# Performance work log

Measured on AMD Instinct MI355X. Metric: run time of the kernel, lower is better.

The kernel has to match this reference:

```python
import jax, jax.numpy as jnp
import numpy as np

B, T, D_IN = 64, 365, 10
D_MODEL, N_HEAD, D_K = 256, 16, 8
D_HEAD = D_MODEL // N_HEAD  # 16, value head dim
MAX_POS = 365 + 2 * 30      # max_position + 2*max_temporal_shift = 425
BN_EPS = 1e-5


def _pos_table(n_pos, d, temp=1000.0):
    # standard sinusoidal table (frozen in the original via Embedding.from_pretrained)
    pos = np.arange(n_pos)[:, None].astype(np.float64)
    i = np.arange(d)[None, :]
    angle = pos / np.power(temp, 2 * (i // 2) / d)
    tab = np.where(i % 2 == 0, np.sin(angle), np.cos(angle))
    return jnp.asarray(tab, jnp.float32)

POS_TABLE = _pos_table(MAX_POS, D_MODEL)


def _linear_layer(x, W, b, g, beta):
    # LinearLayer = Linear -> BatchNorm1d (train-mode batch stats, per-feature) -> ReLU
    y = x @ W.T + b
    ax = tuple(range(y.ndim - 1))
    mu = y.mean(ax, keepdims=True)
    var = y.var(ax, keepdims=True)  # biased var, matches torch BN
    y = (y - mu) * jax.lax.rsqrt(var + BN_EPS) * g + beta
    return jax.nn.relu(y)


def _forward(positions, x, w1, b1, g1, e1, w2, b2, g2, e2, w3, b3, g3, e3,
             ws1, ws2, wi, bi, gi, ei, wk, bk, wq, bq, wm, bm, gm, em,
             wd1, bd1, gd1, ed1, wd2, bd2, gd2, ed2, wc, bc):
    # channel MLP encoder: 10 -> 64 -> 128 -> 256
    out = _linear_layer(x, w1, b1, g1, e1)
    out = _linear_layer(out, w2, b2, g2, e2)
    out = _linear_layer(out, w3, b3, g3, e3)                    # [B,T,256]
    # channel SE attention: avgpool over time, 2 linears (no bias), sigmoid, residual
    pooled = out.mean(axis=1, keepdims=True)                     # [B,1,256]
    att = jax.nn.sigmoid(jax.nn.relu(pooled @ ws1.T) @ ws2.T)    # [B,1,256]
    out = att * pooled + out                                     # broadcast residual
    # temporal attention block
    h = _linear_layer(out, wi, bi, gi, ei)                       # inconv -> [B,T,256]
    e = h + POS_TABLE[positions]                                 # add positional encoding
    q = (e @ wq.T + bq).reshape(B, T, N_HEAD, D_K)
    k = (e @ wk.T + bk).reshape(B, T, N_HEAD, D_K)
    v = e.reshape(B, T, N_HEAD, D_HEAD)
    # 'cross' attention: full score matrix, mean over key dim, softmax over query dim
    scores = jnp.einsum('bthd,bshd->bhts', q, k) / jnp.sqrt(jnp.float32(D_K))  # [B,H,T,T]
    scores = scores.mean(axis=-1)                                # [B,H,T]
    a = jax.nn.softmax(scores, axis=-1)                          # [B,H,T]
    y = jnp.einsum('bht,bthe->bhe', a, v).reshape(B, D_MODEL)    # [B,256]
    y = _linear_layer(y, wm, bm, gm, em)                         # mlp 256 -> 128
    # decoder: 128 -> 64 -> 32 -> num_classes
    z = _linear_layer(y, wd1, bd1, gd1, ed1)
    z = _linear_layer(z, wd2, bd2, gd2, ed2)
    return z @ wc.T + bc                                         # logits [B,10]


def setup_inputs():
    key = jax.random.key(0)
    ks = jax.random.split(key, 16)
    n = lambda i, sh: jax.random.normal(ks[i], sh, jnp.float32) * 0.05
    z, o = jnp.zeros, jnp.ones
    return {
        'x': jax.random.normal(ks[0], (B, T, D_IN), jnp.float32),
        'positions': jnp.sort(jax.random.randint(ks[1], (B, T), 0, MAX_POS), axis=-1),
        'w1': n(2, (64, D_IN)), 'b1': z(64), 'g1': o(64), 'e1': z(64),
        'w2': n(3, (128, 64)), 'b2': z(128), 'g2': o(128), 'e2': z(128),
        'w3': n(4, (256, 128)), 'b3': z(256), 'g3': o(256), 'e3': z(256),
        'ws1': n(5, (16, 256)), 'ws2': n(6, (256, 16)),
        'wi': n(7, (256, 256)), 'bi': z(256), 'gi': o(256), 'ei': z(256),
        'wk': n(8, (128, 256)), 'bk': z(128),
        'wq': n(9, (128, 256)), 'bq': z(128),
        'wm': n(10, (128, 256)), 'bm': z(128), 'gm': o(128), 'em': z(128),
        'wd1': n(11, (64, 128)), 'bd1': z(64), 'gd1': o(64), 'ed1': z(64),
        'wd2': n(12, (32, 64)), 'bd2': z(32), 'gd2': o(32), 'ed2': z(32),
        'wc': n(13, (10, 32)), 'bc': z(10),
    }


def reference(x, positions, w1, b1, g1, e1, w2, b2, g2, e2, w3, b3, g3, e3,
              ws1, ws2, wi, bi, gi, ei, wk, bk, wq, bq, wm, bm, gm, em,
              wd1, bd1, gd1, ed1, wd2, bd2, gd2, ed2, wc, bc):
    return _forward(positions, x, w1, b1, g1, e1, w2, b2, g2, e2, w3, b3, g3, e3,
                    ws1, ws2, wi, bi, gi, ei, wk, bk, wq, bq, wm, bm, gm, em,
                    wd1, bd1, gd1, ed1, wd2, bd2, gd2, ed2, wc, bc)
```

## Files before the change

kernel.cpp:

```cpp
#include <hip/hip_runtime.h>
#include <hip/hip_bf16.h>
#include <math.h>

#define TT 365
#define BT 23360
#define NPOS 425

typedef __hip_bfloat16 bf16;
typedef __attribute__((ext_vector_type(8))) short s16x8;
typedef __attribute__((ext_vector_type(4))) float f32x4;

__device__ __forceinline__ float b2f(bf16 v) { return __bfloat162float(v); }
__device__ __forceinline__ bf16  f2b(float v) { return __float2bfloat16(v); }
__device__ __forceinline__ float u2f(unsigned u) { return __uint_as_float(u); }
__device__ __forceinline__ short f2bs(float v) { bf16 h = __float2bfloat16(v); return *reinterpret_cast<short*>(&h); }
__device__ __forceinline__ void unpack8(uint4 raw, float* v) {
    v[0] = u2f(raw.x << 16); v[1] = u2f(raw.x & 0xffff0000u);
    v[2] = u2f(raw.y << 16); v[3] = u2f(raw.y & 0xffff0000u);
    v[4] = u2f(raw.z << 16); v[5] = u2f(raw.z & 0xffff0000u);
    v[6] = u2f(raw.w << 16); v[7] = u2f(raw.w & 0xffff0000u);
}

__global__ __launch_bounds__(256) void prep_kernel(
    float* __restrict__ stats, float* __restrict__ pooled, float* __restrict__ esum,
    const float* __restrict__ w2, const float* __restrict__ w3, const float* __restrict__ wi,
    const float* __restrict__ wq,
    bf16* __restrict__ whi, bf16* __restrict__ wlo, float* __restrict__ tab)
{
    int i = blockIdx.x * 256 + threadIdx.x;
    if (i < 2048)  { stats[i] = 0.f; return; }  i -= 2048;
    if (i < 16384) { pooled[i] = 0.f; return; } i -= 16384;
    if (i < 16384) { esum[i] = 0.f; return; }   i -= 16384;
    if (i < 139264) {
        float w;
        if      (i < 8192)   w = w2[i];
        else if (i < 40960)  w = w3[i - 8192];
        else if (i < 106496) w = wi[i - 40960];
        else                 w = wq[i - 106496];
        bf16 h = f2b(w);
        whi[i] = h;
        wlo[i] = f2b(w - b2f(h));
        return;
    } i -= 139264;
    if (i < 108800) {
        int c = i & 255, p = i >> 8;
        float e = (float)(2 * (c >> 1)) * (1.f / 256.f);
        float ang = (float)p * exp2f(-e * 9.96578428466209f);
        tab[i] = (c & 1) ? cosf(ang) : sinf(ang);
    }
}

__global__ __launch_bounds__(256) void gemm_l1_kernel(
    const float* __restrict__ x,
    const float* __restrict__ W, const float* __restrict__ bias,
    bf16* __restrict__ Y, float* __restrict__ stats)
{
    const int t  = threadIdx.x;
    const int tx = t & 15, ty = t >> 4;
    const int row0 = blockIdx.x * 64;
    __shared__ float As[64][17];
    __shared__ float Ws[16][65];
    __shared__ float red_s[4][64];
    __shared__ float red_q[4][64];
    float acc[4][4];
#pragma unroll
    for (int rr = 0; rr < 4; ++rr)
#pragma unroll
        for (int cc = 0; cc < 4; ++cc) acc[rr][cc] = 0.f;
#pragma unroll
    for (int i = 0; i < 4; ++i) {
        int idx = t + i * 256, r = idx >> 4, c = idx & 15;
        As[r][c] = (c < 10) ? x[(size_t)(row0 + r) * 10 + c] : 0.f;
    }
#pragma unroll
    for (int i = 0; i < 4; ++i) {
        int idx = t + i * 256, c = idx >> 4, kk = idx & 15;
        Ws[kk][c] = (kk < 10) ? W[(size_t)c * 10 + kk] : 0.f;
    }
    __syncthreads();
#pragma unroll
    for (int kk = 0; kk < 10; ++kk) {
        float a[4];
#pragma unroll
        for (int rr = 0; rr < 4; ++rr) a[rr] = As[ty * 4 + rr][kk];
#pragma unroll
        for (int cc = 0; cc < 4; ++cc) {
            float w = Ws[kk][cc * 16 + tx];
#pragma unroll
            for (int rr = 0; rr < 4; ++rr) acc[rr][cc] = fmaf(a[rr], w, acc[rr][cc]);
        }
    }
    float s_cc[4], q_cc[4];
#pragma unroll
    for (int cc = 0; cc < 4; ++cc) { s_cc[cc] = 0.f; q_cc[cc] = 0.f; }
#pragma unroll
    for (int rr = 0; rr < 4; ++rr) {
        int row = row0 + ty * 4 + rr;
#pragma unroll
        for (int cc = 0; cc < 4; ++cc) {
            int col = cc * 16 + tx;
            float v = acc[rr][cc] + bias[col];
            Y[(size_t)row * 64 + col] = f2b(v);
            s_cc[cc] += v; q_cc[cc] += v * v;
        }
    }
    int w = t >> 6;
#pragma unroll
    for (int cc = 0; cc < 4; ++cc) {
        float s = s_cc[cc], q = q_cc[cc];
        s += __shfl_xor(s, 16); q += __shfl_xor(q, 16);
        s += __shfl_xor(s, 32); q += __shfl_xor(q, 32);
        if ((t & 63) < 16) { red_s[w][cc * 16 + tx] = s; red_q[w][cc * 16 + tx] = q; }
    }
    __syncthreads();
    if (t < 64) {
        float s = red_s[0][t] + red_s[1][t] + red_s[2][t] + red_s[3][t];
        float q = red_q[0][t] + red_q[1][t] + red_q[2][t] + red_q[3][t];
        atomicAdd(&stats[t], s);
        atomicAdd(&stats[256 + t], q);
    }
}

template<int MODE, int K>
__global__ __launch_bounds__(256) void mfma_gemm(
    const bf16* __restrict__ A,
    const bf16* __restrict__ Whi, const bf16* __restrict__ Wlo,
    const float* __restrict__ bias,
    bf16* __restrict__ Y, int ldY, float* __restrict__ stats,
    const float* __restrict__ bnstats, const float* __restrict__ bng,
    const float* __restrict__ bnb, const float* __restrict__ sebuf)
{
    constexpr int KC = (K > 128) ? 128 : K;
    __shared__ s16x8 Wl[2][KC / 8][64];
    __shared__ float red_s[4][64];
    __shared__ float red_q[4][64];
    __shared__ float scb[MODE ? K : 1];
    __shared__ float shb[MODE ? K : 1];
    const int t = threadIdx.x, wave = t >> 6, lane = t & 63;
    const int n16 = lane & 15, quad = lane >> 4;
    const int m0 = blockIdx.x * 64 + wave * 16;
    const int col0 = blockIdx.y * 64;
    const int sc_ = t & 63, skg0 = t >> 6;
    const bf16* gh = Whi + (size_t)(col0 + sc_) * K;
    const bf16* gl = Wlo + (size_t)(col0 + sc_) * K;
#pragma unroll
    for (int kg = skg0; kg < KC / 8; kg += 4) {
        Wl[0][kg][sc_] = *(const s16x8*)(gh + kg * 8);
        Wl[1][kg][sc_] = *(const s16x8*)(gl + kg * 8);
    }
    if (MODE) {
        if (t < K) {
            float mu = bnstats[t] * (1.f / (float)BT);
            float var = bnstats[256 + t] * (1.f / (float)BT) - mu * mu;
            float sc = rsqrtf(var + 1e-5f) * bng[t];
            scb[t] = sc; shb[t] = bnb[t] - mu * sc;
        }
    }
    __syncthreads();
    const int arow = m0 + n16;
    const float* sev = (MODE == 2) ? (sebuf + (arow / TT) * 256) : nullptr;
    const bf16* Ap = A + (size_t)arow * K + quad * 8;
    s16x8 af[K / 32];
#pragma unroll
    for (int i = 0; i < K / 32; ++i) {
        s16x8 raw = *(const s16x8*)(Ap + i * 32);
        if (MODE) {
            int kb = i * 32 + quad * 8;
#pragma unroll
            for (int j = 0; j < 8; ++j) {
                float y = u2f(((unsigned)(unsigned short)raw[j]) << 16);
                float v = fmaxf(fmaf(y, scb[kb + j], shb[kb + j]), 0.f);
                if (MODE == 2) v += sev[kb + j];
                raw[j] = f2bs(v);
            }
        }
        af[i] = raw;
    }
    f32x4 acc[4];
    f32x4 zero = {0.f, 0.f, 0.f, 0.f};
#pragma unroll
    for (int ct = 0; ct < 4; ++ct) acc[ct] = zero;
#pragma unroll
    for (int kc = 0; kc < K; kc += KC) {
        if (kc) {
            __syncthreads();
#pragma unroll
            for (int kg = skg0; kg < KC / 8; kg += 4) {
                Wl[0][kg][sc_] = *(const s16x8*)(gh + kc + kg * 8);
                Wl[1][kg][sc_] = *(const s16x8*)(gl + kc + kg * 8);
            }
            __syncthreads();
        }
#pragma unroll
        for (int i = 0; i < KC / 32; ++i) {
            const int kgq = i * 4 + quad;
            const s16x8 a = af[(kc >> 5) + i];
#pragma unroll
            for (int ct = 0; ct < 4; ++ct) {
                s16x8 bl = Wl[1][kgq][ct * 16 + n16];
                s16x8 bh = Wl[0][kgq][ct * 16 + n16];
                acc[ct] = __builtin_amdgcn_mfma_f32_16x16x32_bf16(a, bl, acc[ct], 0, 0, 0);
                acc[ct] = __builtin_amdgcn_mfma_f32_16x16x32_bf16(a, bh, acc[ct], 0, 0, 0);
            }
        }
    }
#pragma unroll
    for (int ct = 0; ct < 4; ++ct) {
        int col = col0 + ct * 16 + n16;
        float bv = bias[col];
        float s = 0.f, q = 0.f;
#pragma unroll
        for (int r = 0; r < 4; ++r) {
            float v = acc[ct][r] + bv;
            int row = m0 + quad * 4 + r;
            Y[(size_t)row * ldY + col] = f2b(v);
            s += v; q += v * v;
        }
        s += __shfl_xor(s, 16); q += __shfl_xor(q, 16);
        s += __shfl_xor(s, 32); q += __shfl_xor(q, 32);
        if (quad == 0) { red_s[wave][ct * 16 + n16] = s; red_q[wave][ct * 16 + n16] = q; }
    }
    if (stats) {
        __syncthreads();
        if (t < 64) {
            float s = red_s[0][t] + red_s[1][t] + red_s[2][t] + red_s[3][t];
            float q = red_q[0][t] + red_q[1][t] + red_q[2][t] + red_q[3][t];
            atomicAdd(&stats[col0 + t], s);
            atomicAdd(&stats[256 + col0 + t], q);
        }
    }
}

__global__ __launch_bounds__(256) void pool_partial_kernel(
    const bf16* __restrict__ Y3, const float* __restrict__ stats,
    const float* __restrict__ g3, const float* __restrict__ e3,
    float* __restrict__ pooled)
{
    const int b = blockIdx.x, part = blockIdx.y, t = threadIdx.x;
    const int cg = t & 31, rs = t >> 5;
    __shared__ float scb[256], shb[256];
    __shared__ float pp[8][256];
    {
        float mu = stats[t] * (1.f / (float)BT);
        float var = stats[256 + t] * (1.f / (float)BT) - mu * mu;
        float sc = rsqrtf(var + 1e-5f) * g3[t];
        scb[t] = sc; shb[t] = e3[t] - mu * sc;
    }
    __syncthreads();
    float acc[8] = {0.f,0.f,0.f,0.f,0.f,0.f,0.f,0.f};
    const int r0 = part * 46;
#pragma unroll
    for (int i = 0; i < 6; ++i) {
        int l = rs + i * 8;
        int r = r0 + l;
        if (l < 46 && r < TT) {
            uint4 raw = *(const uint4*)(Y3 + ((size_t)b * TT + r) * 256 + cg * 8);
            float v[8];
            unpack8(raw, v);
#pragma unroll
            for (int j = 0; j < 8; ++j)
                acc[j] += fmaxf(fmaf(v[j], scb[cg * 8 + j], shb[cg * 8 + j]), 0.f);
        }
    }
#pragma unroll
    for (int j = 0; j < 8; ++j) pp[rs][cg * 8 + j] = acc[j];
    __syncthreads();
    float s = 0.f;
#pragma unroll
    for (int r = 0; r < 8; ++r) s += pp[r][t];
    atomicAdd(&pooled[b * 256 + t], s);
}

__global__ __launch_bounds__(256) void esum_kernel(const bf16* __restrict__ e,
                                                   float* __restrict__ esum)
{
    const int b = blockIdx.x, part = blockIdx.y, t = threadIdx.x;
    const int cg = t & 31, rs = t >> 5;
    __shared__ float pp[8][256];
    float acc[8] = {0.f,0.f,0.f,0.f,0.f,0.f,0.f,0.f};
    const int r0 = part * 46;
#pragma unroll
    for (int i = 0; i < 6; ++i) {
        int l = rs + i * 8;
        int r = r0 + l;
        if (l < 46 && r < TT) {
            uint4 raw = *(const uint4*)(e + ((size_t)b * TT + r) * 256 + cg * 8);
            float v[8];
            unpack8(raw, v);
#pragma unroll
            for (int j = 0; j < 8; ++j) acc[j] += v[j];
        }
    }
#pragma unroll
    for (int j = 0; j < 8; ++j) pp[rs][cg * 8 + j] = acc[j];
    __syncthreads();
    float s = 0.f;
#pragma unroll
    for (int r = 0; r < 8; ++r) s += pp[r][t];
    atomicAdd(&esum[b * 256 + t], s);
}

__global__ __launch_bounds__(256) void se_mlp_kernel(const float* __restrict__ pooled,
                                                     const float* __restrict__ ws1,
                                                     const float* __restrict__ ws2,
                                                     float* __restrict__ se) {
    int b = blockIdx.x, f = threadIdx.x;
    __shared__ float pl[256];
    __shared__ float hidden[16];
    float p = pooled[b * 256 + f] * (1.f / (float)TT);
    pl[f] = p;
    __syncthreads();
    if (f < 16) {
        float h = 0.f;
        for (int k2 = 0; k2 < 256; ++k2) h = fmaf(pl[k2], ws1[f * 256 + k2], h);
        hidden[f] = fmaxf(h, 0.f);
    }
    __syncthreads();
    float a = 0.f;
    for (int k2 = 0; k2 < 16; ++k2) a = fmaf(hidden[k2], ws2[f * 16 + k2], a);
    a = 1.f / (1.f + expf(-a));
    se[b * 256 + f] = a * p;
}

__global__ __launch_bounds__(256) void bnrelu8_kernel(
    const bf16* __restrict__ Y, const float* __restrict__ stats,
    const float* __restrict__ g, const float* __restrict__ beta,
    bf16* __restrict__ Out, const float* __restrict__ tab, const int* __restrict__ pos) {
    int i = (blockIdx.x * 256 + threadIdx.x) * 8;
    int col = i & 255, row = i >> 8;
    uint4 raw = *(const uint4*)(Y + i);
    float v[8];
    unpack8(raw, v);
    const float invM = 1.f / (float)BT;
    const float* tr = tab + pos[row] * 256 + col;
    bf16 tmp[8] __attribute__((aligned(16)));
#pragma unroll
    for (int j = 0; j < 8; ++j) {
        float mu  = stats[col + j] * invM;
        float var = stats[256 + col + j] * invM - mu * mu;
        float o = (v[j] - mu) * rsqrtf(var + 1e-5f) * g[col + j] + beta[col + j];
        tmp[j] = f2b(fmaxf(o, 0.f) + tr[j]);
    }
    *(uint4*)(Out + i) = *(const uint4*)tmp;
}

__global__ __launch_bounds__(64) void attn_kernel(
    const bf16* __restrict__ q, const bf16* __restrict__ e,
    const float* __restrict__ esum, const float* __restrict__ wk,
    const float* __restrict__ bk, float* __restrict__ yv)
{
    __shared__ float aw[368];
    const int b = blockIdx.x, h = blockIdx.y;
    const int lane = threadIdx.x;
    float4 es = *(const float4*)(esum + b * 256 + lane * 4);
    float ks[8];
#pragma unroll
    for (int d = 0; d < 8; ++d) {
        float4 wv = *(const float4*)(wk + (size_t)(h * 8 + d) * 256 + lane * 4);
        ks[d] = es.x * wv.x + es.y * wv.y + es.z * wv.z + es.w * wv.w;
    }
#pragma unroll
    for (int off = 1; off < 64; off <<= 1)
#pragma unroll
        for (int d = 0; d < 8; ++d) ks[d] += __shfl_xor(ks[d], off);
#pragma unroll
    for (int d = 0; d < 8; ++d) ks[d] += (float)TT * bk[h * 8 + d];
    const float scale = 1.f / (sqrtf(8.f) * (float)TT);
    const bf16* qb = q + (size_t)b * TT * 128 + h * 8;
    float sv[6];
    float m = -1e30f;
#pragma unroll
    for (int i = 0; i < 6; ++i) {
        int r = lane + i * 64;
        float s = -1e30f;
        if (r < TT) {
            uint4 raw = *(const uint4*)(qb + (size_t)r * 128);
            float v[8];
            unpack8(raw, v);
            float dot = 0.f;
#pragma unroll
            for (int j = 0; j < 8; ++j) dot = fmaf(v[j], ks[j], dot);
            s = dot * scale;
        }
        sv[i] = s;
        m = fmaxf(m, s);
    }
#pragma unroll
    for (int off = 1; off < 64; off <<= 1) m = fmaxf(m, __shfl_xor(m, off));
    float sum = 0.f;
#pragma unroll
    for (int i = 0; i < 6; ++i) {
        float ev = (sv[i] > -1e29f) ? expf(sv[i] - m) : 0.f;
        sv[i] = ev; sum += ev;
    }
#pragma unroll
    for (int off = 1; off < 64; off <<= 1) sum += __shfl_xor(sum, off);
    float inv = 1.f / sum;
#pragma unroll
    for (int i = 0; i < 6; ++i) {
        int r = lane + i * 64;
        if (r < TT) aw[r] = sv[i] * inv;
    }
    __syncthreads();
    const int half = lane & 1, rs = lane >> 1;
    float acc[8] = {0.f,0.f,0.f,0.f,0.f,0.f,0.f,0.f};
    const bf16* ebase = e + (size_t)b * TT * 256 + h * 16 + half * 8;
#pragma unroll
    for (int i = 0; i < 12; ++i) {
        int r = rs + i * 32;
        if (r < TT) {
            uint4 raw = *(const uint4*)(ebase + (size_t)r * 256);
            float v[8];
            unpack8(raw, v);
            float a = aw[r];
#pragma unroll
            for (int j = 0; j < 8; ++j) acc[j] = fmaf(a, v[j], acc[j]);
        }
    }
#pragma unroll
    for (int off = 2; off < 64; off <<= 1)
#pragma unroll
        for (int j = 0; j < 8; ++j) acc[j] += __shfl_xor(acc[j], off);
    if (lane < 2) {
        float* op = yv + b * 256 + h * 16 + half * 8;
#pragma unroll
        for (int j = 0; j < 8; ++j) op[j] = acc[j];
    }
}

__global__ __launch_bounds__(1024) void tail_kernel(
    const float* __restrict__ yv,
    const float* wm, const float* bm, const float* gm, const float* em,
    const float* wd1, const float* bd1, const float* gd1, const float* ed1,
    const float* wd2, const float* bd2, const float* gd2, const float* ed2,
    const float* wc, const float* bc, float* __restrict__ out)
{
    __shared__ float lds[12352];
    const int t = threadIdx.x;
    const int r = t & 63, cg = t >> 6;
    float* Xq  = lds;
    float* Wp  = lds + 4160;
    float* Z1t = lds;
    float* Wd1h = lds + 8192;
    float* Z2t = lds;
    float* Wd2 = lds + 4096;
    float* Z3t = lds + 6144;
    float* WcL = lds + 8192;

    float acc1[8] = {0.f,0.f,0.f,0.f,0.f,0.f,0.f,0.f};
    const int c01 = cg * 8;
    for (int p = 0; p < 4; ++p) {
        __syncthreads();
        for (int i = t; i < 4096; i += 1024) {
            int kk = i & 63, rr = i >> 6;
            Xq[kk * 65 + rr] = yv[rr * 256 + p * 64 + kk];
        }
        {
            const float4* wm4 = (const float4*)wm;
            float4* Wp4 = (float4*)Wp;
            for (int i = t; i < 2048; i += 1024) {
                int kk4 = i & 15, c = i >> 4;
                Wp4[c * 16 + kk4] = wm4[c * 64 + p * 16 + kk4];
            }
        }
        __syncthreads();
#pragma unroll 4
        for (int k4 = 0; k4 < 16; ++k4) {
            float xv[4];
#pragma unroll
            for (int j = 0; j < 4; ++j) xv[j] = Xq[(k4 * 4 + j) * 65 + r];
#pragma unroll
            for (int c = 0; c < 8; ++c) {
                float4 w = *(const float4*)(Wp + (c01 + c) * 64 + k4 * 4);
                acc1[c] = fmaf(xv[0], w.x, acc1[c]);
                acc1[c] = fmaf(xv[1], w.y, acc1[c]);
                acc1[c] = fmaf(xv[2], w.z, acc1[c]);
                acc1[c] = fmaf(xv[3], w.w, acc1[c]);
            }
        }
    }
    float z1v[8];
#pragma unroll
    for (int c = 0; c < 8; ++c) {
        float v = acc1[c] + bm[c01 + c];
        float s = v, q = v * v;
#pragma unroll
        for (int off = 1; off < 64; off <<= 1) { s += __shfl_xor(s, off); q += __shfl_xor(q, off); }
        float mu = s * (1.f / 64.f), var = q * (1.f / 64.f) - mu * mu;
        z1v[c] = fmaxf((v - mu) * rsqrtf(var + 1e-5f) * gm[c01 + c] + em[c01 + c], 0.f);
    }
    __syncthreads();
#pragma unroll
    for (int c = 0; c < 8; ++c) Z1t[(c01 + c) * 64 + r] = z1v[c];
    float acc2[4] = {0.f, 0.f, 0.f, 0.f};
    const int c02 = cg * 4;
    for (int ph = 0; ph < 2; ++ph) {
        __syncthreads();
        {
            const float4* s4 = (const float4*)wd1;
            float4* d4 = (float4*)Wd1h;
            int kk4 = t & 15, c = t >> 4;
            d4[c * 16 + kk4] = s4[c * 32 + ph * 16 + kk4];
        }
        __syncthreads();
#pragma unroll 4
        for (int k4 = 0; k4 < 16; ++k4) {
            float xv[4];
#pragma unroll
            for (int j = 0; j < 4; ++j) xv[j] = Z1t[(ph * 64 + k4 * 4 + j) * 64 + r];
#pragma unroll
            for (int c = 0; c < 4; ++c) {
                float4 w = *(const float4*)(Wd1h + (c02 + c) * 64 + k4 * 4);
                acc2[c] = fmaf(xv[0], w.x, acc2[c]);
                acc2[c] = fmaf(xv[1], w.y, acc2[c]);
                acc2[c] = fmaf(xv[2], w.z, acc2[c]);
                acc2[c] = fmaf(xv[3], w.w, acc2[c]);
            }
        }
    }
    float z2v[4];
#pragma unroll
    for (int c = 0; c < 4; ++c) {
        float v = acc2[c] + bd1[c02 + c];
        float s = v, q = v * v;
#pragma unroll
        for (int off = 1; off < 64; off <<= 1) { s += __shfl_xor(s, off); q += __shfl_xor(q, off); }
        float mu = s * (1.f / 64.f), var = q * (1.f / 64.f) - mu * mu;
        z2v[c] = fmaxf((v - mu) * rsqrtf(var + 1e-5f) * gd1[c02 + c] + ed1[c02 + c], 0.f);
    }
    __syncthreads();
#pragma unroll
    for (int c = 0; c < 4; ++c) Z2t[(c02 + c) * 64 + r] = z2v[c];
    {
        const float4* s4 = (const float4*)wd2;
        float4* d4 = (float4*)Wd2;
        if (t < 512) d4[t] = s4[t];
    }
    __syncthreads();
    float acc3[2] = {0.f, 0.f};
    const int c03 = cg * 2;
#pragma unroll 4
    for (int k4 = 0; k4 < 16; ++k4) {
        float xv[4];
#pragma unroll
        for (int j = 0; j < 4; ++j) xv[j] = Z2t[(k4 * 4 + j) * 64 + r];
#pragma unroll
        for (int c = 0; c < 2; ++c) {
            float4 w = *(const float4*)(Wd2 + (c03 + c) * 64 + k4 * 4);
            acc3[c] = fmaf(xv[0], w.x, acc3[c]);
            acc3[c] = fmaf(xv[1], w.y, acc3[c]);
            acc3[c] = fmaf(xv[2], w.z, acc3[c]);
            acc3[c] = fmaf(xv[3], w.w, acc3[c]);
        }
    }
#pragma unroll
    for (int c = 0; c < 2; ++c) {
        float v = acc3[c] + bd2[c03 + c];
        float s = v, q = v * v;
#pragma unroll
        for (int off = 1; off < 64; off <<= 1) { s += __shfl_xor(s, off); q += __shfl_xor(q, off); }
        float mu = s * (1.f / 64.f), var = q * (1.f / 64.f) - mu * mu;
        Z3t[(c03 + c) * 64 + r] = fmaxf((v - mu) * rsqrtf(var + 1e-5f) * gd2[c03 + c] + ed2[c03 + c], 0.f);
    }
    if (t < 80) ((float4*)WcL)[t] = ((const float4*)wc)[t];
    __syncthreads();
    if (t < 640) {
        int rr = t / 10, c = t % 10;
        float s = bc[c];
#pragma unroll
        for (int kk = 0; kk < 32; ++kk) s = fmaf(Z3t[kk * 64 + rr], WcL[c * 32 + kk], s);
        out[t] = s;
    }
}


extern "C" void kernel_launch(void* const* d_in, const int* in_sizes, int n_in,
                              void* d_out, int out_size, void* d_ws, size_t ws_size,
                              hipStream_t stream) {
    (void)in_sizes; (void)n_in; (void)out_size; (void)ws_size;
    const float* x  = (const float*)d_in[0];
    const int* pos  = (const int*)d_in[1];
    const float *w1 = (const float*)d_in[2],  *b1 = (const float*)d_in[3],
                *g1 = (const float*)d_in[4],  *e1 = (const float*)d_in[5];
    const float *w2 = (const float*)d_in[6],  *b2 = (const float*)d_in[7],
                *g2 = (const float*)d_in[8],  *e2 = (const float*)d_in[9];
    const float *w3 = (const float*)d_in[10], *b3 = (const float*)d_in[11],
                *g3 = (const float*)d_in[12], *e3 = (const float*)d_in[13];
    const float *ws1 = (const float*)d_in[14], *ws2 = (const float*)d_in[15];
    const float *wi = (const float*)d_in[16], *bi = (const float*)d_in[17],
                *gi = (const float*)d_in[18], *ei = (const float*)d_in[19];
    const float *wk = (const float*)d_in[20], *bk = (const float*)d_in[21];
    const float *wq = (const float*)d_in[22], *bq = (const float*)d_in[23];
    const float *wm = (const float*)d_in[24], *bm = (const float*)d_in[25],
                *gm = (const float*)d_in[26], *em = (const float*)d_in[27];
    const float *wd1 = (const float*)d_in[28], *bd1 = (const float*)d_in[29],
                *gd1 = (const float*)d_in[30], *ed1 = (const float*)d_in[31];
    const float *wd2 = (const float*)d_in[32], *bd2 = (const float*)d_in[33],
                *gd2 = (const float*)d_in[34], *ed2 = (const float*)d_in[35];
    const float *wc = (const float*)d_in[36], *bc = (const float*)d_in[37];
    float* out = (float*)d_out;

    char* w8 = (char*)d_ws;
    bf16*  actA   = (bf16*)(w8);
    bf16*  actB   = (bf16*)(w8 + 11960320);
    bf16*  whi    = (bf16*)(w8 + 23920640);
    bf16*  wlo    = (bf16*)(w8 + 24199168);
    float* tab    = (float*)(w8 + 24477696);
    float* stats  = (float*)(w8 + 24912896);
    float* pooled = (float*)(w8 + 24921088);
    float* sebuf  = (float*)(w8 + 24986624);
    float* esum   = (float*)(w8 + 25052160);
    float* yvb    = (float*)(w8 + 25117696);

    prep_kernel<<<1105, 256, 0, stream>>>(stats, pooled, esum, w2, w3, wi, wq, whi, wlo, tab);
    gemm_l1_kernel<<<365, 256, 0, stream>>>(x, w1, b1, actB, stats);
    mfma_gemm<1, 64><<<dim3(365, 2), 256, 0, stream>>>(actB, whi, wlo, b2,
                                                       actA, 128, stats + 512, stats, g1, e1, nullptr);
    mfma_gemm<1, 128><<<dim3(365, 4), 256, 0, stream>>>(actA, whi + 8192, wlo + 8192, b3,
                                                        actB, 256, stats + 1024, stats + 512, g2, e2, nullptr);
    pool_partial_kernel<<<dim3(64, 8), 256, 0, stream>>>(actB, stats + 1024, g3, e3, pooled);
    se_mlp_kernel<<<64, 256, 0, stream>>>(pooled, ws1, ws2, sebuf);
    mfma_gemm<2, 256><<<dim3(365, 4), 256, 0, stream>>>(actB, whi + 40960, wlo + 40960, bi,
                                                        actA, 256, stats + 1536, stats + 1024, g3, e3, sebuf);
    bnrelu8_kernel<<<BT * 256 / 2048, 256, 0, stream>>>(actA, stats + 1536, gi, ei, actB, tab, pos);
    esum_kernel<<<dim3(64, 8), 256, 0, stream>>>(actB, esum);
    mfma_gemm<0, 256><<<dim3(365, 2), 256, 0, stream>>>(actB, whi + 106496, wlo + 106496, bq,
                                                        actA, 128, nullptr, nullptr, nullptr, nullptr, nullptr);
    attn_kernel<<<dim3(64, 16), 64, 0, stream>>>(actA, actB, esum, wk, bk, yvb);
    tail_kernel<<<1, 1024, 0, stream>>>(yvb, wm, bm, gm, em, wd1, bd1, gd1, ed1,
                                        wd2, bd2, gd2, ed2, wc, bc, out);
}
```

Baseline: 318.6 us.

## Replace BN stat atomics with per-block partials and a reduction kernel

Each GEMM now writes its per-block column sums and sums of squares to a partials buffer instead of issuing atomicAdds. A new single-block reduction kernel turns these into BN scale/shift coefficients, so downstream kernels load precomputed coefficients rather than recomputing mean/var per thread. The tail kernel also drops its LDS weight staging and reads weights straight from global memory with wider unrolling. This trades atomic contention and redundant rsqrt work for four extra serial launches, each with a small single-block kernel.

Measured after the change: 395.1 us. 1.24x slower.

```diff
diff --git a/kernel.cpp b/kernel.cpp
--- a/kernel.cpp
+++ b/kernel.cpp
@@ -22,13 +22,12 @@
 }
 
 __global__ __launch_bounds__(256) void prep_kernel(
-    float* __restrict__ stats, float* __restrict__ pooled, float* __restrict__ esum,
+    float* __restrict__ pooled, float* __restrict__ esum,
     const float* __restrict__ w2, const float* __restrict__ w3, const float* __restrict__ wi,
     const float* __restrict__ wq,
     bf16* __restrict__ whi, bf16* __restrict__ wlo, float* __restrict__ tab)
 {
     int i = blockIdx.x * 256 + threadIdx.x;
-    if (i < 2048)  { stats[i] = 0.f; return; }  i -= 2048;
     if (i < 16384) { pooled[i] = 0.f; return; } i -= 16384;
     if (i < 16384) { esum[i] = 0.f; return; }   i -= 16384;
     if (i < 139264) {
@@ -50,10 +49,34 @@
     }
 }
 
+__global__ __launch_bounds__(512) void red_kernel(
+    const float* __restrict__ partials, const float* __restrict__ g,
+    const float* __restrict__ beta, float* __restrict__ coef, int Ncols)
+{
+    __shared__ float sums[512];
+    const int t = threadIdx.x;
+    const int c = t & 255;
+    const int off = (t >> 8) << 8;
+    float s = 0.f;
+    if (c < Ncols) {
+        const float* p = partials + off + c;
+        for (int r = 0; r < 365; ++r) s += p[r * 512];
+    }
+    sums[t] = s;
+    __syncthreads();
+    if (t < Ncols) {
+        float mu = sums[t] * (1.f / (float)BT);
+        float var = sums[256 + t] * (1.f / (float)BT) - mu * mu;
+        float sc = rsqrtf(var + 1e-5f) * g[t];
+        coef[t] = sc;
+        coef[256 + t] = beta[t] - mu * sc;
+    }
+}
+
 __global__ __launch_bounds__(256) void gemm_l1_kernel(
     const float* __restrict__ x,
     const float* __restrict__ W, const float* __restrict__ bias,
-    bf16* __restrict__ Y, float* __restrict__ stats)
+    bf16* __restrict__ Y, float* __restrict__ partials)
 {
     const int t  = threadIdx.x;
     const int tx = t & 15, ty = t >> 4;
@@ -114,10 +137,9 @@
     }
     __syncthreads();
     if (t < 64) {
-        float s = red_s[0][t] + red_s[1][t] + red_s[2][t] + red_s[3][t];
-        float q = red_q[0][t] + red_q[1][t] + red_q[2][t] + red_q[3][t];
-        atomicAdd(&stats[t], s);
-        atomicAdd(&stats[256 + t], q);
+        float* pr = partials + (size_t)blockIdx.x * 512;
+        pr[t]       = red_s[0][t] + red_s[1][t] + red_s[2][t] + red_s[3][t];
+        pr[256 + t] = red_q[0][t] + red_q[1][t] + red_q[2][t] + red_q[3][t];
     }
 }
 
@@ -126,9 +148,8 @@
     const bf16* __restrict__ A,
     const bf16* __restrict__ Whi, const bf16* __restrict__ Wlo,
     const float* __restrict__ bias,
-    bf16* __restrict__ Y, int ldY, float* __restrict__ stats,
-    const float* __restrict__ bnstats, const float* __restrict__ bng,
-    const float* __restrict__ bnb, const float* __restrict__ sebuf)
+    bf16* __restrict__ Y, int ldY, float* __restrict__ partials,
+    const float* __restrict__ coef, const float* __restrict__ sebuf)
 {
     constexpr int KC = (K > 128) ? 128 : K;
     __shared__ s16x8 Wl[2][KC / 8][64];
@@ -149,12 +170,7 @@
         Wl[1][kg][sc_] = *(const s16x8*)(gl + kg * 8);
     }
     if (MODE) {
-        if (t < K) {
-            float mu = bnstats[t] * (1.f / (float)BT);
-            float var = bnstats[256 + t] * (1.f / (float)BT) - mu * mu;
-            float sc = rsqrtf(var + 1e-5f) * bng[t];
-            scb[t] = sc; shb[t] = bnb[t] - mu * sc;
-        }
+        if (t < K) { scb[t] = coef[t]; shb[t] = coef[256 + t]; }
     }
     __syncthreads();
     const int arow = m0 + n16;
@@ -220,32 +236,25 @@
         s += __shfl_xor(s, 32); q += __shfl_xor(q, 32);
         if (quad == 0) { red_s[wave][ct * 16 + n16] = s; red_q[wave][ct * 16 + n16] = q; }
     }
-    if (stats) {
+    if (partials) {
         __syncthreads();
         if (t < 64) {
-            float s = red_s[0][t] + red_s[1][t] + red_s[2][t] + red_s[3][t];
-            float q = red_q[0][t] + red_q[1][t] + red_q[2][t] + red_q[3][t];
-            atomicAdd(&stats[col0 + t], s);
-            atomicAdd(&stats[256 + col0 + t], q);
+            float* pr = partials + (size_t)blockIdx.x * 512;
+            pr[col0 + t]       = red_s[0][t] + red_s[1][t] + red_s[2][t] + red_s[3][t];
+            pr[256 + col0 + t] = red_q[0][t] + red_q[1][t] + red_q[2][t] + red_q[3][t];
         }
     }
 }
 
 __global__ __launch_bounds__(256) void pool_partial_kernel(
-    const bf16* __restrict__ Y3, const float* __restrict__ stats,
-    const float* __restrict__ g3, const float* __restrict__ e3,
+    const bf16* __restrict__ Y3, const float* __restrict__ coef,
     float* __restrict__ pooled)
 {
     const int b = blockIdx.x, part = blockIdx.y, t = threadIdx.x;
     const int cg = t & 31, rs = t >> 5;
     __shared__ float scb[256], shb[256];
     __shared__ float pp[8][256];
-    {
-        float mu = stats[t] * (1.f / (float)BT);
-        float var = stats[256 + t] * (1.f / (float)BT) - mu * mu;
-        float sc = rsqrtf(var + 1e-5f) * g3[t];
-        scb[t] = sc; shb[t] = e3[t] - mu * sc;
-    }
+    scb[t] = coef[t]; shb[t] = coef[256 + t];
     __syncthreads();
     float acc[8] = {0.f,0.f,0.f,0.f,0.f,0.f,0.f,0.f};
     const int r0 = part * 46;
@@ -323,22 +332,18 @@
 }
 
 __global__ __launch_bounds__(256) void bnrelu8_kernel(
-    const bf16* __restrict__ Y, const float* __restrict__ stats,
-    const float* __restrict__ g, const float* __restrict__ beta,
+    const bf16* __restrict__ Y, const float* __restrict__ coef,
     bf16* __restrict__ Out, const float* __restrict__ tab, const int* __restrict__ pos) {
     int i = (blockIdx.x * 256 + threadIdx.x) * 8;
     int col = i & 255, row = i >> 8;
     uint4 raw = *(const uint4*)(Y + i);
     float v[8];
     unpack8(raw, v);
-    const float invM = 1.f / (float)BT;
     const float* tr = tab + pos[row] * 256 + col;
     bf16 tmp[8] __attribute__((aligned(16)));
 #pragma unroll
     for (int j = 0; j < 8; ++j) {
-        float mu  = stats[col + j] * invM;
-        float var = stats[256 + col + j] * invM - mu * mu;
-        float o = (v[j] - mu) * rsqrtf(var + 1e-5f) * g[col + j] + beta[col + j];
+        float o = fmaf(v[j], coef[col + j], coef[256 + col + j]);
         tmp[j] = f2b(fmaxf(o, 0.f) + tr[j]);
     }
     *(uint4*)(Out + i) = *(const uint4*)tmp;
@@ -430,145 +435,115 @@
 
 __global__ __launch_bounds__(1024) void tail_kernel(
     const float* __restrict__ yv,
-    const float* wm, const float* bm, const float* gm, const float* em,
-    const float* wd1, const float* bd1, const float* gd1, const float* ed1,
-    const float* wd2, const float* bd2, const float* gd2, const float* ed2,
-    const float* wc, const float* bc, float* __restrict__ out)
+    const float* __restrict__ wm, const float* __restrict__ bm,
+    const float* __restrict__ gm, const float* __restrict__ em,
+    const float* __restrict__ wd1, const float* __restrict__ bd1,
+    const float* __restrict__ gd1, const float* __restrict__ ed1,
+    const float* __restrict__ wd2, const float* __restrict__ bd2,
+    const float* __restrict__ gd2, const float* __restrict__ ed2,
+    const float* __restrict__ wc, const float* __restrict__ bc,
+    float* __restrict__ out)
 {
     __shared__ float lds[12352];
+    float* Xq  = lds;
+    float* Z1t = lds + 4160;
+    float* Z2t = lds;
+    float* Z3t = lds + 4160;
     const int t = threadIdx.x;
     const int r = t & 63, cg = t >> 6;
-    float* Xq  = lds;
-    float* Wp  = lds + 4160;
-    float* Z1t = lds;
-    float* Wd1h = lds + 8192;
-    float* Z2t = lds;
-    float* Wd2 = lds + 4096;
-    float* Z3t = lds + 6144;
-    float* WcL = lds + 8192;
+    const int cgu = __builtin_amdgcn_readfirstlane(cg);
 
     float acc1[8] = {0.f,0.f,0.f,0.f,0.f,0.f,0.f,0.f};
-    const int c01 = cg * 8;
     for (int p = 0; p < 4; ++p) {
         __syncthreads();
         for (int i = t; i < 4096; i += 1024) {
             int kk = i & 63, rr = i >> 6;
             Xq[kk * 65 + rr] = yv[rr * 256 + p * 64 + kk];
         }
-        {
-            const float4* wm4 = (const float4*)wm;
-            float4* Wp4 = (float4*)Wp;
-            for (int i = t; i < 2048; i += 1024) {
-                int kk4 = i & 15, c = i >> 4;
-                Wp4[c * 16 + kk4] = wm4[c * 64 + p * 16 + kk4];
+        __syncthreads();
+        const float* wb = wm + (size_t)(cgu * 8) * 256 + p * 64;
+#pragma unroll
+        for (int kg = 0; kg < 4; ++kg) {
+            float xv[16];
+#pragma unroll
+            for (int j = 0; j < 16; ++j) xv[j] = Xq[(kg * 16 + j) * 65 + r];
+#pragma unroll
+            for (int c = 0; c < 8; ++c) {
+                const float* wp = wb + c * 256 + kg * 16;
+#pragma unroll
+                for (int j = 0; j < 16; ++j) acc1[c] = fmaf(xv[j], wp[j], acc1[c]);
             }
         }
-        __syncthreads();
-#pragma unroll 4
-        for (int k4 = 0; k4 < 16; ++k4) {
-            float xv[4];
-#pragma unroll
-            for (int j = 0; j < 4; ++j) xv[j] = Xq[(k4 * 4 + j) * 65 + r];
-#pragma unroll
-            for (int c = 0; c < 8; ++c) {
-                float4 w = *(const float4*)(Wp + (c01 + c) * 64 + k4 * 4);
-                acc1[c] = fmaf(xv[0], w.x, acc1[c]);
-                acc1[c] = fmaf(xv[1], w.y, acc1[c]);
-                acc1[c] = fmaf(xv[2], w.z, acc1[c]);
-                acc1[c] = fmaf(xv[3], w.w, acc1[c]);
-            }
-        }
     }
     float z1v[8];
 #pragma unroll
     for (int c = 0; c < 8; ++c) {
-        float v = acc1[c] + bm[c01 + c];
+        float v = acc1[c] + bm[cgu * 8 + c];
         float s = v, q = v * v;
 #pragma unroll
         for (int off = 1; off < 64; off <<= 1) { s += __shfl_xor(s, off); q += __shfl_xor(q, off); }
         float mu = s * (1.f / 64.f), var = q * (1.f / 64.f) - mu * mu;
-        z1v[c] = fmaxf((v - mu) * rsqrtf(var + 1e-5f) * gm[c01 + c] + em[c01 + c], 0.f);
-    }
-    __syncthreads();
-#pragma unroll
-    for (int c = 0; c < 8; ++c) Z1t[(c01 + c) * 64 + r] = z1v[c];
+        z1v[c] = fmaxf((v - mu) * rsqrtf(var + 1e-5f) * gm[cgu * 8 + c] + em[cgu * 8 + c], 0.f);
+    }
+    __syncthreads();
+#pragma unroll
+    for (int c = 0; c < 8; ++c) Z1t[(cgu * 8 + c) * 64 + r] = z1v[c];
+    __syncthreads();
     float acc2[4] = {0.f, 0.f, 0.f, 0.f};
-    const int c02 = cg * 4;
-    for (int ph = 0; ph < 2; ++ph) {
-        __syncthreads();
-        {
-            const float4* s4 = (const float4*)wd1;
-            float4* d4 = (float4*)Wd1h;
-            int kk4 = t & 15, c = t >> 4;
-            d4[c * 16 + kk4] = s4[c * 32 + ph * 16 + kk4];
-        }
-        __syncthreads();
-#pragma unroll 4
-        for (int k4 = 0; k4 < 16; ++k4) {
-            float xv[4];
-#pragma unroll
-            for (int j = 0; j < 4; ++j) xv[j] = Z1t[(ph * 64 + k4 * 4 + j) * 64 + r];
-#pragma unroll
-            for (int c = 0; c < 4; ++c) {
-                float4 w = *(const float4*)(Wd1h + (c02 + c) * 64 + k4 * 4);
-                acc2[c] = fmaf(xv[0], w.x, acc2[c]);
-                acc2[c] = fmaf(xv[1], w.y, acc2[c]);
-                acc2[c] = fmaf(xv[2], w.z, acc2[c]);
-                acc2[c] = fmaf(xv[3], w.w, acc2[c]);
-            }
+#pragma unroll
+    for (int kg = 0; kg < 8; ++kg) {
+        float xv[16];
+#pragma unroll
+        for (int j = 0; j < 16; ++j) xv[j] = Z1t[(kg * 16 + j) * 64 + r];
+#pragma unroll
+        for (int c = 0; c < 4; ++c) {
+            const float* wp = wd1 + (size_t)(cgu * 4 + c) * 128 + kg * 16;
+#pragma unroll
+            for (int j = 0; j < 16; ++j) acc2[c] = fmaf(xv[j], wp[j], acc2[c]);
         }
     }
     float z2v[4];
 #pragma unroll
     for (int c = 0; c < 4; ++c) {
-        float v = acc2[c] + bd1[c02 + c];
+        float v = acc2[c] + bd1[cgu * 4 + c];
         float s = v, q = v * v;
 #pragma unroll
         for (int off = 1; off < 64; off <<= 1) { s += __shfl_xor(s, off); q += __shfl_xor(q, off); }
         float mu = s * (1.f / 64.f), var = q * (1.f / 64.f) - mu * mu;
-        z2v[c] = fmaxf((v - mu) * rsqrtf(var + 1e-5f) * gd1[c02 + c] + ed1[c02 + c], 0.f);
-    }
-    __syncthreads();
-#pragma unroll
-    for (int c = 0; c < 4; ++c) Z2t[(c02 + c) * 64 + r] = z2v[c];
-    {
-        const float4* s4 = (const float4*)wd2;
-        float4* d4 = (float4*)Wd2;
-        if (t < 512) d4[t] = s4[t];
-    }
+        z2v[c] = fmaxf((v - mu) * rsqrtf(var + 1e-5f) * gd1[cgu * 4 + c] + ed1[cgu * 4 + c], 0.f);
+    }
+    __syncthreads();
+#pragma unroll
+    for (int c = 0; c < 4; ++c) Z2t[(cgu * 4 + c) * 64 + r] = z2v[c];
     __syncthreads();
     float acc3[2] = {0.f, 0.f};
-    const int c03 = cg * 2;
-#pragma unroll 4
-    for (int k4 = 0; k4 < 16; ++k4) {
-        float xv[4];
-#pragma unroll
-        for (int j = 0; j < 4; ++j) xv[j] = Z2t[(k4 * 4 + j) * 64 + r];
+#pragma unroll
+    for (int kg = 0; kg < 4; ++kg) {
+        float xv[16];
+#pragma unroll
+        for (int j = 0; j < 16; ++j) xv[j] = Z2t[(kg * 16 + j) * 64 + r];
 #pragma unroll
         for (int c = 0; c < 2; ++c) {
-            float4 w = *(const float4*)(Wd2 + (c03 + c) * 64 + k4 * 4);
-            acc3[c] = fmaf(xv[0], w.x, acc3[c]);
-            acc3[c] = fmaf(xv[1], w.y, acc3[c]);
-            acc3[c] = fmaf(xv[2], w.z, acc3[c]);
-            acc3[c] = fmaf(xv[3], w.w, acc3[c]);
+            const float* wp = wd2 + (size_t)(cgu * 2 + c) * 64 + kg * 16;
+#pragma unroll
+            for (int j = 0; j < 16; ++j) acc3[c] = fmaf(xv[j], wp[j], acc3[c]);
         }
     }
 #pragma unroll
     for (int c = 0; c < 2; ++c) {
-        float v = acc3[c] + bd2[c03 + c];
+        float v = acc3[c] + bd2[cgu * 2 + c];
         float s = v, q = v * v;
 #pragma unroll
         for (int off = 1; off < 64; off <<= 1) { s += __shfl_xor(s, off); q += __shfl_xor(q, off); }
         float mu = s * (1.f / 64.f), var = q * (1.f / 64.f) - mu * mu;
-        Z3t[(c03 + c) * 64 + r] = fmaxf((v - mu) * rsqrtf(var + 1e-5f) * gd2[c03 + c] + ed2[c03 + c], 0.f);
-    }
-    if (t < 80) ((float4*)WcL)[t] = ((const float4*)wc)[t];
+        Z3t[(cgu * 2 + c) * 64 + r] = fmaxf((v - mu) * rsqrtf(var + 1e-5f) * gd2[cgu * 2 + c] + ed2[cgu * 2 + c], 0.f);
+    }
     __syncthreads();
     if (t < 640) {
         int rr = t / 10, c = t % 10;
         float s = bc[c];
 #pragma unroll
-        for (int kk = 0; kk < 32; ++kk) s = fmaf(Z3t[kk * 64 + rr], WcL[c * 32 + kk], s);
+        for (int kk = 0; kk < 32; ++kk) s = fmaf(Z3t[kk * 64 + rr], wc[c * 32 + kk], s);
         out[t] = s;
     }
 }
@@ -606,26 +581,31 @@
     bf16*  whi    = (bf16*)(w8 + 23920640);
     bf16*  wlo    = (bf16*)(w8 + 24199168);
     float* tab    = (float*)(w8 + 24477696);
-    float* stats  = (float*)(w8 + 24912896);
-    float* pooled = (float*)(w8 + 24921088);
-    float* sebuf  = (float*)(w8 + 24986624);
-    float* esum   = (float*)(w8 + 25052160);
-    float* yvb    = (float*)(w8 + 25117696);
-
-    prep_kernel<<<1105, 256, 0, stream>>>(stats, pooled, esum, w2, w3, wi, wq, whi, wlo, tab);
-    gemm_l1_kernel<<<365, 256, 0, stream>>>(x, w1, b1, actB, stats);
+    float* parts  = (float*)(w8 + 24912896);
+    float* coef   = (float*)(w8 + 25660416);
+    float* pooled = (float*)(w8 + 25668608);
+    float* sebuf  = (float*)(w8 + 25734144);
+    float* esum   = (float*)(w8 + 25799680);
+    float* yvb    = (float*)(w8 + 25865216);
+
+    prep_kernel<<<1097, 256, 0, stream>>>(pooled, esum, w2, w3, wi, wq, whi, wlo, tab);
+    gemm_l1_kernel<<<365, 256, 0, stream>>>(x, w1, b1, actB, parts);
+    red_kernel<<<1, 512, 0, stream>>>(parts, g1, e1, coef, 64);
     mfma_gemm<1, 64><<<dim3(365, 2), 256, 0, stream>>>(actB, whi, wlo, b2,
-                                                       actA, 128, stats + 512, stats, g1, e1, nullptr);
+                                                       actA, 128, parts, coef, nullptr);
+    red_kernel<<<1, 512, 0, stream>>>(parts, g2, e2, coef + 512, 128);
     mfma_gemm<1, 128><<<dim3(365, 4), 256, 0, stream>>>(actA, whi + 8192, wlo + 8192, b3,
-                                                        actB, 256, stats + 1024, stats + 512, g2, e2, nullptr);
-    pool_partial_kernel<<<dim3(64, 8), 256, 0, stream>>>(actB, stats + 1024, g3, e3, pooled);
+                                                        actB, 256, parts, coef + 512, nullptr);
+    red_kernel<<<1, 512, 0, stream>>>(parts, g3, e3, coef + 1024, 256);
+    pool_partial_kernel<<<dim3(64, 8), 256, 0, stream>>>(actB, coef + 1024, pooled);
     se_mlp_kernel<<<64, 256, 0, stream>>>(pooled, ws1, ws2, sebuf);
     mfma_gemm<2, 256><<<dim3(365, 4), 256, 0, stream>>>(actB, whi + 40960, wlo + 40960, bi,
-                                                        actA, 256, stats + 1536, stats + 1024, g3, e3, sebuf);
-    bnrelu8_kernel<<<BT * 256 / 2048, 256, 0, stream>>>(actA, stats + 1536, gi, ei, actB, tab, pos);
+                                                        actA, 256, parts, coef + 1024, sebuf);
+    red_kernel<<<1, 512, 0, stream>>>(parts, gi, ei, coef + 1536, 256);
+    bnrelu8_kernel<<<BT * 256 / 2048, 256, 0, stream>>>(actA, coef + 1536, actB, tab, pos);
     esum_kernel<<<dim3(64, 8), 256, 0, stream>>>(actB, esum);
     mfma_gemm<0, 256><<<dim3(365, 2), 256, 0, stream>>>(actB, whi + 106496, wlo + 106496, bq,
-                                                        actA, 128, nullptr, nullptr, nullptr, nullptr, nullptr);
+                                                        actA, 128, nullptr, nullptr, nullptr);
     attn_kernel<<<dim3(64, 16), 64, 0, stream>>>(actA, actB, esum, wk, bk, yvb);
     tail_kernel<<<1, 1024, 0, stream>>>(yvb, wm, bm, gm, em, wd1, bd1, gd1, ed1,
                                         wd2, bd2, gd2, ed2, wc, bc, out);
```
